# Performance work log

Hardware: AMD Instinct MI355X
Metric: run time of the kernel (lower is better)

Reference implementation:

```python
import jax, jax.numpy as jnp
import numpy as np

# ---- fixed config (Linear_mvm defaults, XBAR 64x64) ----
ROW = 64; COL = 64
BIT_SLICE = 2; BIT_STREAM = 1
W_BITS = 16; W_FRAC = 12          # weight_bit_frac = weight_bits//4*3
I_BITS = 16; I_FRAC = 12          # input_bit_frac  = input_bits//4*3
ADC_BIT = 8                       # log2(ROW) + bit_slice (bit_stream==1)
ACM_BITS = 16; ACM_FRAC = 12
BSN = W_BITS // BIT_SLICE         # 8 slices per weight, MSB-first columns
STN = I_BITS // BIT_STREAM        # 16 input bit-streams, LSB-first
IN_F = 1024; OUT_F = 1024; BATCH = 256


def _bit_slice_weight(w_nonneg):
    # w_nonneg: [out, in] nonnegative -> sliced crossbar matrix [in, out*BSN] (MSB->LSB per channel)
    w_int = jnp.clip(jnp.round(w_nonneg * (2.0 ** W_FRAC)), 0.0, 2.0 ** W_BITS - 1.0)
    shifts = (BIT_SLICE * (BSN - 1 - jnp.arange(BSN))).astype(jnp.float32)
    sl = jnp.floor(w_int[..., None] / (2.0 ** shifts)) % (2 ** BIT_SLICE)  # [out,in,BSN]
    o, i = w_nonneg.shape
    return sl.transpose(1, 0, 2).reshape(i, o * BSN)


def _input_bits(x):
    # two's-complement fixed point, LSB-first bit planes: [b, in, STN]
    x_int = jnp.clip(jnp.round(x * (2.0 ** I_FRAC)), -(2.0 ** (I_BITS - 1)), 2.0 ** (I_BITS - 1) - 1.0)
    x_u = jnp.where(x_int < 0, x_int + 2.0 ** I_BITS, x_int)
    return jnp.floor(x_u[..., None] / (2.0 ** jnp.arange(I_BITS, dtype=jnp.float32))) % 2.0


def _tile(mat, r, c):
    # pad to tile multiples and reshape to [xr, xc, r, c]
    pr = (-mat.shape[0]) % r; pc = (-mat.shape[1]) % c
    m = jnp.pad(mat, ((0, pr), (0, pc)))
    xr, xc = m.shape[0] // r, m.shape[1] // c
    return m.reshape(xr, r, xc, c).transpose(0, 2, 1, 3)


def _adc(a):
    # uniform ADC quantization of the analog column current to ADC_BIT bits
    full = float(ROW * (2 ** BIT_SLICE - 1))
    step = full / (2.0 ** ADC_BIT - 1.0)
    return jnp.clip(jnp.round(a / step) * step, 0.0, full)


def _mvm_one_sign(bits_tiled, xbars):
    # bits_tiled [b, xr, ROW, STN]; xbars [xr, xc, ROW, COL]
    sw_slice = 2.0 ** (BIT_SLICE * (BSN - 1 - jnp.arange(BSN, dtype=jnp.float32)))  # MSB..LSB
    sw_stream = 2.0 ** (BIT_STREAM * jnp.arange(STN, dtype=jnp.float32))
    sw_stream = sw_stream.at[-1].multiply(-1.0)  # two's-complement MSB stream

    def step(acc, si):
        bi, w = si                                   # bi [b,xr,ROW]
        analog = jnp.einsum('brk,rckj->brcj', bi, xbars)  # [b,xr,xc,COL]
        analog = _adc(analog)
        b, xr, xc, _ = analog.shape
        dig = analog.reshape(b, xr, xc, COL // BSN, BSN) @ sw_slice  # shift-add slices
        return acc + w * dig, None

    b = bits_tiled.shape[0]; xr, xc = xbars.shape[0], xbars.shape[1]
    acc0 = jnp.zeros((b, xr, xc, COL // BSN), jnp.float32)
    streams = jnp.moveaxis(bits_tiled, -1, 0)  # [STN, b, xr, ROW]
    acc, _ = jax.lax.scan(step, acc0, (streams, sw_stream))
    return acc.sum(axis=1).reshape(b, xc * (COL // BSN))  # sum row tiles, flatten channels


def _forward(x, weight, bias):
    pos = _bit_slice_weight(jnp.maximum(weight, 0.0))
    neg = _bit_slice_weight(-jnp.minimum(weight, 0.0))
    xb_pos = _tile(pos, ROW, COL)
    xb_neg = _tile(neg, ROW, COL)
    bits = _input_bits(x)                                  # [b,in,STN]
    xr = xb_pos.shape[0]
    bits = jnp.pad(bits, ((0, 0), (0, xr * ROW - bits.shape[1]), (0, 0)))
    bits = bits.reshape(x.shape[0], xr, ROW, STN)
    out = _mvm_one_sign(bits, xb_pos) - _mvm_one_sign(bits, xb_neg)
    out = out * (2.0 ** (-(W_FRAC + I_FRAC)))              # undo fixed-point scaling
    # accumulator quantization to ACM_BITS / ACM_FRAC
    out = jnp.clip(jnp.round(out * 2.0 ** ACM_FRAC), -(2.0 ** (ACM_BITS - 1)), 2.0 ** (ACM_BITS - 1) - 1.0) * 2.0 ** (-ACM_FRAC)
    out = out[:, :OUT_F]
    return out + bias[None, :]


def setup_inputs() -> dict:
    key = jax.random.key(0)
    k1, k2, k3 = jax.random.split(key, 3)
    x = jax.random.normal(k1, (BATCH, IN_F), jnp.float32)
    weight = jax.random.normal(k2, (OUT_F, IN_F), jnp.float32) * 0.05  # representable in Q4.12
    bias = jax.random.normal(k3, (OUT_F,), jnp.float32) * 0.05
    return {"x": x, "weight": weight, "bias": bias}


def reference(x, weight, bias):
    return _forward(x, weight, bias)
```

## Files before the change

### kernel.cpp

```cpp
#include <hip/hip_runtime.h>
#include <stdint.h>

#define BATCH 256
#define IN_F  1024
#define OUT_F 1024
#define RT    16
#define STN   16
#define NCOL  16384

typedef int   v4i  __attribute__((ext_vector_type(4)));
typedef int   v16i __attribute__((ext_vector_type(16)));
typedef float v2f  __attribute__((ext_vector_type(2)));

#define AP_SZ ((size_t)STN * BATCH * IN_F)
#define BP_SZ ((size_t)64 * NCOL * 16)

__global__ __launch_bounds__(256) void pack_fused(
    const float* __restrict__ x, const float* __restrict__ w,
    uint8_t* __restrict__ Ap2, uint8_t* __restrict__ Bp,
    uint32_t* __restrict__ flags)
{
    if (blockIdx.x < 512) {
        int item = blockIdx.x * 256 + threadIdx.x;
        int g  = item & 63;
        int o  = (item >> 6) & 1023;
        int sg = item >> 16;
        const float* wr = w + (size_t)o * IN_F + g * 16;
        uint32_t wq[16];
        #pragma unroll
        for (int j = 0; j < 16; ++j) {
            float wv = wr[j];
            float wf = rintf(fmaxf(sg ? -wv : wv, 0.0f) * 4096.0f);
            wq[j] = (uint32_t)fminf(wf, 65535.0f);
        }
        #pragma unroll
        for (int s = 0; s < 8; ++s) {
            int sh = 14 - 2 * s;
            uint32_t dw[4], nz = 0;
            #pragma unroll
            for (int q = 0; q < 4; ++q) {
                uint32_t d = 0;
                #pragma unroll
                for (int j = 0; j < 4; ++j)
                    d |= ((wq[q * 4 + j] >> sh) & 3u) << (8 * j);
                dw[q] = d;
                nz |= d;
            }
            int sgs = sg * 8 + s;
            *(uint4*)(Bp + (size_t)(g * NCOL + sgs * 1024 + o) * 16) =
                make_uint4(dw[0], dw[1], dw[2], dw[3]);
            unsigned long long bal = __ballot((int)(nz != 0));
            if ((threadIdx.x & 63) == 0 && bal) {
                unsigned long long t = bal | (bal >> 1);
                t |= t >> 2;
                t &= 0x1111111111111111ULL;
                uint32_t r16 = 0;
                #pragma unroll
                for (int i = 0; i < 16; ++i)
                    r16 |= (uint32_t)((t >> (4 * i)) & 1ULL) << i;
                atomicOr(&flags[sgs * 32 + (o >> 5)], r16);
            }
        }
    } else {
        int item = (blockIdx.x - 512) * 256 + threadIdx.x;
        int kg = item & 63;
        int tq = (item >> 6) & 3;
        int b  = item >> 8;
        int r = kg >> 2, f = (kg >> 1) & 1, hi = kg & 1;
        int y = b >> 5, l16 = hi * 32 + (b & 31);
        const float* xr = x + (size_t)b * IN_F + kg * 16;
        uint32_t xu[16];
        #pragma unroll
        for (int j = 0; j < 16; ++j) {
            float xf = rintf(xr[j] * 4096.0f);
            xf = fminf(fmaxf(xf, -32768.0f), 32767.0f);
            xu[j] = (uint32_t)((int)xf) & 0xFFFFu;
        }
        uint8_t* wbase = Ap2 + ((size_t)(r * 8 + y) * 16) * 2048 + f * 1024 + l16 * 16;
        #pragma unroll
        for (int tt = 0; tt < 4; ++tt) {
            int t = tq * 4 + tt;
            uint32_t dw[4];
            #pragma unroll
            for (int q = 0; q < 4; ++q) {
                uint32_t d = 0;
                #pragma unroll
                for (int j = 0; j < 4; ++j)
                    d |= ((xu[q * 4 + j] >> t) & 1u) << (8 * j);
                dw[q] = d;
            }
            *(uint4*)(wbase + t * 2048) = make_uint4(dw[0], dw[1], dw[2], dw[3]);
        }
    }
}

__global__ __launch_bounds__(1024, 4) void cim_block(
    const uint8_t* __restrict__ Ap2, const uint8_t* __restrict__ Bp,
    const uint32_t* __restrict__ flags, const float* __restrict__ bias,
    float* __restrict__ out)
{
    __shared__ float red[16 * 1024];
    const float MAG = 12582912.0f;
    int tid = threadIdx.x, wid = tid >> 6, l = tid & 63, h2 = l >> 5;
    int oq = blockIdx.x, y = blockIdx.y;

    uint32_t fw = flags[(l & 15) * 32 + oq];
    uint32_t rmask = fw;
    #pragma unroll
    for (int st = 1; st < 16; st <<= 1)
        rmask |= __shfl_xor(rmask, st, 64);

    v2f acc2[8];
    #pragma unroll
    for (int i = 0; i < 8; ++i) acc2[i] = (v2f)0.0f;
    v16i zero;
    #pragma unroll
    for (int i = 0; i < 16; ++i) zero[i] = 0;

    int cnt = 0;
    uint32_t rm = rmask;
    while (rm) {
        int r = __builtin_ctz(rm);
        rm &= rm - 1;
        uint32_t smask = (uint32_t)__ballot((int)((fw >> r) & 1u)) & 0xFFFFu;
        while (smask) {
            int sgs = __builtin_ctz(smask);
            smask &= smask - 1;
            if ((cnt++ & 15) != wid) continue;

            int s = sgs & 7, sg = sgs >> 3;
            float clane = __int_as_float((141 - 2 * s) << 23) * (192.0f / 255.0f);
            if (sg) clane = -clane;
            int col = sgs * 1024 + oq * 32 + (l & 31);

            v4i bf0 = *(const v4i*)(Bp + ((size_t)(r * 4 + h2)     * NCOL + col) * 16);
            v4i bf1 = *(const v4i*)(Bp + ((size_t)(r * 4 + 2 + h2) * NCOL + col) * 16);

            const uint8_t* abase = Ap2 + (size_t)(r * 8 + y) * 32768 + l * 16;
            #pragma unroll 4
            for (int t = 0; t < STN; ++t) {
                v4i af0 = *(const v4i*)(abase + t * 2048);
                v4i af1 = *(const v4i*)(abase + t * 2048 + 1024);
                v16i c = __builtin_amdgcn_mfma_i32_32x32x32_i8(af0, bf0, zero, 0, 0, 0);
                c      = __builtin_amdgcn_mfma_i32_32x32x32_i8(af1, bf1, c,    0, 0, 0);
                float wt = (t == 15) ? -32768.0f : (float)(1 << t);
                float cw = clane * wt;
                #pragma unroll
                for (int i = 0; i < 8; ++i) {
                    v2f af; af.x = (float)c[2 * i]; af.y = (float)c[2 * i + 1];
                    v2f tq;
                    tq.x = fmaf(af.x, 1.328125f, MAG);
                    tq.y = fmaf(af.y, 1.328125f, MAG);
                    v2f qf = tq - MAG;
                    acc2[i].x = fmaf(qf.x, cw, acc2[i].x);
                    acc2[i].y = fmaf(qf.y, cw, acc2[i].y);
                }
            }
        }
    }

    #pragma unroll
    for (int i = 0; i < 16; ++i) {
        float v = (i & 1) ? acc2[i >> 1].y : acc2[i >> 1].x;
        red[wid * 1024 + i * 64 + l] = v;
    }
    __syncthreads();
    {
        int i = wid;
        float v = 0.0f;
        #pragma unroll
        for (int w16 = 0; w16 < 16; ++w16) v += red[w16 * 1024 + i * 64 + l];
        int b = y * 32 + (i & 3) + 8 * (i >> 2) + 4 * h2;
        int o = oq * 32 + (l & 31);
        float ov = v * 0x1p-24f;
        float q = rintf(ov * 4096.0f);
        q = fminf(fmaxf(q, -32768.0f), 32767.0f);
        out[(size_t)b * OUT_F + o] = q * 0x1p-12f + bias[o];
    }
}

extern "C" void kernel_launch(void* const* d_in, const int* in_sizes, int n_in,
                              void* d_out, int out_size, void* d_ws, size_t ws_size,
                              hipStream_t stream) {
    const float* x    = (const float*)d_in[0];
    const float* w    = (const float*)d_in[1];
    const float* bias = (const float*)d_in[2];
    float* out = (float*)d_out;

    uint8_t*  Ap2   = (uint8_t*)d_ws;
    uint8_t*  Bp    = Ap2 + AP_SZ;
    uint32_t* flags = (uint32_t*)(Bp + BP_SZ);

    hipMemsetAsync(flags, 0, 512 * sizeof(uint32_t), stream);
    hipLaunchKernelGGL(pack_fused, dim3(768), dim3(256), 0, stream,
                       x, w, Ap2, Bp, flags);
    hipLaunchKernelGGL(cim_block, dim3(32, 8), dim3(1024), 0, stream,
                       Ap2, Bp, flags, bias, out);
}
```

Measured before the change: 165.5 us.

## Switch CIM kernel to 16x16x64 MFMA tiles with more, smaller blocks

Replaces the 32x32x32 int8 MFMA pair with a single 16x16x64 MFMA per bit-stream. Blocks become 16x16 output tiles of 512 threads, giving a 64x16 grid instead of 32x8, which raises parallelism and cuts accumulator registers and shared memory. The atomicOr flag accumulation and the memset are replaced by plain per-column mask stores, which each block ORs together when it loads them. In exchange, the crossbar-tile loop and mask reads are repeated across more blocks, and the finer granularity may reduce reuse of A and B loads.

```diff
diff --git a/kernel.cpp b/kernel.cpp
--- a/kernel.cpp
+++ b/kernel.cpp
@@ -9,7 +9,6 @@
 #define NCOL  16384
 
 typedef int   v4i  __attribute__((ext_vector_type(4)));
-typedef int   v16i __attribute__((ext_vector_type(16)));
 typedef float v2f  __attribute__((ext_vector_type(2)));
 
 #define AP_SZ ((size_t)STN * BATCH * IN_F)
@@ -18,7 +17,7 @@
 __global__ __launch_bounds__(256) void pack_fused(
     const float* __restrict__ x, const float* __restrict__ w,
     uint8_t* __restrict__ Ap2, uint8_t* __restrict__ Bp,
-    uint32_t* __restrict__ flags)
+    uint32_t* __restrict__ rmask)
 {
     if (blockIdx.x < 512) {
         int item = blockIdx.x * 256 + threadIdx.x;
@@ -50,7 +49,7 @@
             *(uint4*)(Bp + (size_t)(g * NCOL + sgs * 1024 + o) * 16) =
                 make_uint4(dw[0], dw[1], dw[2], dw[3]);
             unsigned long long bal = __ballot((int)(nz != 0));
-            if ((threadIdx.x & 63) == 0 && bal) {
+            if ((threadIdx.x & 63) == 0) {
                 unsigned long long t = bal | (bal >> 1);
                 t |= t >> 2;
                 t &= 0x1111111111111111ULL;
@@ -58,7 +57,7 @@
                 #pragma unroll
                 for (int i = 0; i < 16; ++i)
                     r16 |= (uint32_t)((t >> (4 * i)) & 1ULL) << i;
-                atomicOr(&flags[sgs * 32 + (o >> 5)], r16);
+                rmask[sgs * 1024 + o] = r16;
             }
         }
     } else {
@@ -94,31 +93,36 @@
     }
 }
 
-__global__ __launch_bounds__(1024, 4) void cim_block(
+__global__ __launch_bounds__(512, 8) void cim16(
     const uint8_t* __restrict__ Ap2, const uint8_t* __restrict__ Bp,
-    const uint32_t* __restrict__ flags, const float* __restrict__ bias,
+    const uint32_t* __restrict__ rmask, const float* __restrict__ bias,
     float* __restrict__ out)
 {
-    __shared__ float red[16 * 1024];
+    __shared__ float red[8 * 256];
     const float MAG = 12582912.0f;
-    int tid = threadIdx.x, wid = tid >> 6, l = tid & 63, h2 = l >> 5;
-    int oq = blockIdx.x, y = blockIdx.y;
+    int tid = threadIdx.x, wid = tid >> 6, l = tid & 63;
+    int oq = blockIdx.x, yb = blockIdx.y;
+    int y32 = yb >> 1, h = yb & 1;
+    int kg = l >> 4, cl = l & 15;
 
-    uint32_t fw = flags[(l & 15) * 32 + oq];
-    uint32_t rmask = fw;
+    const uint4* rm4 = (const uint4*)(rmask + (l & 15) * 1024 + oq * 16);
+    uint4 m0 = rm4[0], m1 = rm4[1], m2 = rm4[2], m3 = rm4[3];
+    uint32_t fw = m0.x | m0.y | m0.z | m0.w | m1.x | m1.y | m1.z | m1.w
+                | m2.x | m2.y | m2.z | m2.w | m3.x | m3.y | m3.z | m3.w;
+    uint32_t rmu = fw;
     #pragma unroll
     for (int st = 1; st < 16; st <<= 1)
-        rmask |= __shfl_xor(rmask, st, 64);
+        rmu |= __shfl_xor(rmu, st, 64);
 
-    v2f acc2[8];
-    #pragma unroll
-    for (int i = 0; i < 8; ++i) acc2[i] = (v2f)0.0f;
-    v16i zero;
-    #pragma unroll
-    for (int i = 0; i < 16; ++i) zero[i] = 0;
+    int aoff = (kg >> 1) * 1024 + ((kg & 1) * 32 + h * 16 + cl) * 16;
+
+    v2f acc2[2];
+    acc2[0] = (v2f)0.0f; acc2[1] = (v2f)0.0f;
+    v4i zero4;
+    zero4[0] = 0; zero4[1] = 0; zero4[2] = 0; zero4[3] = 0;
 
     int cnt = 0;
-    uint32_t rm = rmask;
+    uint32_t rm = rmu;
     while (rm) {
         int r = __builtin_ctz(rm);
         rm &= rm - 1;
@@ -126,31 +130,28 @@
         while (smask) {
             int sgs = __builtin_ctz(smask);
             smask &= smask - 1;
-            if ((cnt++ & 15) != wid) continue;
+            if ((cnt++ & 7) != wid) continue;
 
             int s = sgs & 7, sg = sgs >> 3;
             float clane = __int_as_float((141 - 2 * s) << 23) * (192.0f / 255.0f);
             if (sg) clane = -clane;
-            int col = sgs * 1024 + oq * 32 + (l & 31);
 
-            v4i bf0 = *(const v4i*)(Bp + ((size_t)(r * 4 + h2)     * NCOL + col) * 16);
-            v4i bf1 = *(const v4i*)(Bp + ((size_t)(r * 4 + 2 + h2) * NCOL + col) * 16);
+            v4i bf = *(const v4i*)(Bp +
+                ((size_t)(r * 4 + kg) * NCOL + sgs * 1024 + oq * 16 + cl) * 16);
+            const uint8_t* ab = Ap2 + (size_t)(r * 8 + y32) * 32768 + aoff;
 
-            const uint8_t* abase = Ap2 + (size_t)(r * 8 + y) * 32768 + l * 16;
             #pragma unroll 4
             for (int t = 0; t < STN; ++t) {
-                v4i af0 = *(const v4i*)(abase + t * 2048);
-                v4i af1 = *(const v4i*)(abase + t * 2048 + 1024);
-                v16i c = __builtin_amdgcn_mfma_i32_32x32x32_i8(af0, bf0, zero, 0, 0, 0);
-                c      = __builtin_amdgcn_mfma_i32_32x32x32_i8(af1, bf1, c,    0, 0, 0);
+                v4i af = *(const v4i*)(ab + t * 2048);
+                v4i c = __builtin_amdgcn_mfma_i32_16x16x64_i8(af, bf, zero4, 0, 0, 0);
                 float wt = (t == 15) ? -32768.0f : (float)(1 << t);
                 float cw = clane * wt;
                 #pragma unroll
-                for (int i = 0; i < 8; ++i) {
-                    v2f af; af.x = (float)c[2 * i]; af.y = (float)c[2 * i + 1];
+                for (int i = 0; i < 2; ++i) {
+                    v2f af2; af2.x = (float)c[2 * i]; af2.y = (float)c[2 * i + 1];
                     v2f tq;
-                    tq.x = fmaf(af.x, 1.328125f, MAG);
-                    tq.y = fmaf(af.y, 1.328125f, MAG);
+                    tq.x = fmaf(af2.x, 1.328125f, MAG);
+                    tq.y = fmaf(af2.y, 1.328125f, MAG);
                     v2f qf = tq - MAG;
                     acc2[i].x = fmaf(qf.x, cw, acc2[i].x);
                     acc2[i].y = fmaf(qf.y, cw, acc2[i].y);
@@ -160,22 +161,22 @@
     }
 
     #pragma unroll
-    for (int i = 0; i < 16; ++i) {
+    for (int i = 0; i < 4; ++i) {
         float v = (i & 1) ? acc2[i >> 1].y : acc2[i >> 1].x;
-        red[wid * 1024 + i * 64 + l] = v;
+        red[wid * 256 + i * 64 + l] = v;
     }
     __syncthreads();
-    {
-        int i = wid;
+    if (tid < 256) {
+        int le = tid & 63, ie = tid >> 6;
         float v = 0.0f;
         #pragma unroll
-        for (int w16 = 0; w16 < 16; ++w16) v += red[w16 * 1024 + i * 64 + l];
-        int b = y * 32 + (i & 3) + 8 * (i >> 2) + 4 * h2;
-        int o = oq * 32 + (l & 31);
+        for (int w8 = 0; w8 < 8; ++w8) v += red[w8 * 256 + ie * 64 + le];
+        int row = (le >> 4) * 4 + ie;
+        int o = oq * 16 + (le & 15);
         float ov = v * 0x1p-24f;
         float q = rintf(ov * 4096.0f);
         q = fminf(fmaxf(q, -32768.0f), 32767.0f);
-        out[(size_t)b * OUT_F + o] = q * 0x1p-12f + bias[o];
+        out[(size_t)(yb * 16 + row) * OUT_F + o] = q * 0x1p-12f + bias[o];
     }
 }
 
@@ -189,11 +190,10 @@
 
     uint8_t*  Ap2   = (uint8_t*)d_ws;
     uint8_t*  Bp    = Ap2 + AP_SZ;
-    uint32_t* flags = (uint32_t*)(Bp + BP_SZ);
+    uint32_t* rmask = (uint32_t*)(Bp + BP_SZ);
 
-    hipMemsetAsync(flags, 0, 512 * sizeof(uint32_t), stream);
     hipLaunchKernelGGL(pack_fused, dim3(768), dim3(256), 0, stream,
-                       x, w, Ap2, Bp, flags);
-    hipLaunchKernelGGL(cim_block, dim3(32, 8), dim3(1024), 0, stream,
-                       Ap2, Bp, flags, bias, out);
+                       x, w, Ap2, Bp, rmask);
+    hipLaunchKernelGGL(cim16, dim3(64, 16), dim3(512), 0, stream,
+                       Ap2, Bp, rmask, bias, out);
 }
```

After: 164.2 us. About the same (-0.8%).
